# Optimization experiments

Measured on AMD Instinct MI355X. Metric: run time of the kernel, lower is better.

The kernel has to match this reference:

```python
import jax, jax.numpy as jnp
import numpy as np

IMG_LEN, TXT_LEN = 50, 76
SEQ = IMG_LEN + TXT_LEN
D_IMG, D, VOCAB = 768, 512, 49408
N_LAYERS = 2
EPS = 1e-5


def _layer_norm(x, g, b):
    m = jnp.mean(x, axis=-1, keepdims=True)
    v = jnp.mean(jnp.square(x - m), axis=-1, keepdims=True)
    return (x - m) * jax.lax.rsqrt(v + EPS) * g + b


def setup_inputs() -> dict:
    key = jax.random.key(0)
    ks = jax.random.split(key, 20)
    s = 0.02
    inp = {
        "image_embeddings": jax.random.normal(ks[0], (32, IMG_LEN, D_IMG), jnp.float32),
        "caption_ids": jax.random.randint(ks[1], (32, TXT_LEN), 0, VOCAB),
        "token_emb": jax.random.normal(ks[2], (VOCAB, D), jnp.float32) * s,
        "pos_emb": jax.random.normal(ks[3], (TXT_LEN, D), jnp.float32) * s,
        "ff0_w": jax.random.normal(ks[4], (D_IMG, D), jnp.float32) * s,
        "ff0_b": jnp.zeros((D,), jnp.float32),
        "wq": jax.random.normal(ks[5], (D, D), jnp.float32) * s,
        "wq_b": jnp.zeros((D,), jnp.float32),
        "wk": jax.random.normal(ks[6], (D, D), jnp.float32) * s,
        "wk_b": jnp.zeros((D,), jnp.float32),
        "wv": jax.random.normal(ks[7], (D, D), jnp.float32) * s,
        "wv_b": jnp.zeros((D,), jnp.float32),
        "ln_g": jnp.ones((D,), jnp.float32),
        "ln_b": jnp.zeros((D,), jnp.float32),
        "ff1_w": jax.random.normal(ks[8], (D, D), jnp.float32) * s,
        "ff1_b": jnp.zeros((D,), jnp.float32),
        "ff2_w": jax.random.normal(ks[9], (D, VOCAB), jnp.float32) * s,
        "ff2_b": jnp.zeros((VOCAB,), jnp.float32),
    }
    return inp


def reference(image_embeddings, caption_ids, token_emb, pos_emb, ff0_w, ff0_b,
              wq, wq_b, wk, wk_b, wv, wv_b, ln_g, ln_b, ff1_w, ff1_b, ff2_w, ff2_b):
    # prefix-causal mask: fully visible image prefix, causal over the rest
    mask = jnp.tril(jnp.ones((SEQ, SEQ), jnp.float32)).at[:, :IMG_LEN].set(1.0)

    img = image_embeddings @ ff0_w + ff0_b                      # [B,50,512]
    txt = token_emb[caption_ids] + pos_emb[None, :, :]          # [B,76,512]
    x = jnp.concatenate([img, txt], axis=1)                     # [B,126,512]
    x = _layer_norm(x, ln_g, ln_b)

    for _ in range(N_LAYERS):  # shared params across layers (as in source)
        res1 = x
        q = x @ wq + wq_b
        k = x @ wk + wk_b
        v = x @ wv + wv_b
        sims = jnp.einsum('bqd,bkd->bqk', q, k) / np.sqrt(D).astype(np.float32)
        sims = jnp.where(mask == 0, -1e9, sims)
        attn = jax.nn.softmax(sims, axis=-1)
        x = jnp.einsum('bqk,bkd->bqd', attn, v)
        x = _layer_norm(x + res1, ln_g, ln_b)
        res2 = x
        x = x @ ff1_w + ff1_b
        x = _layer_norm(x + res2, ln_g, ln_b)

    logits = x @ ff2_w + ff2_b                                  # [B,126,VOCAB]
    return logits[:, IMG_LEN:, :]                               # [B,76,VOCAB]
```

## Files before the change

kernel.cpp:

```cpp
#include <hip/hip_runtime.h>

typedef unsigned short ushort_t;
typedef __attribute__((ext_vector_type(8))) short short8;
typedef __attribute__((ext_vector_type(4))) float f32x4;
typedef __attribute__((ext_vector_type(4))) unsigned short bf4;
typedef __attribute__((ext_vector_type(8))) unsigned short bf8v;

__device__ __forceinline__ ushort_t f2bf(float f) {
    union { float f; unsigned u; } v; v.f = f;
    unsigned r = v.u + 0x7FFFu + ((v.u >> 16) & 1u);
    return (ushort_t)(r >> 16);
}

__device__ __forceinline__ void g2lds16(const ushort_t* g, ushort_t* l) {
    __builtin_amdgcn_global_load_lds(
        (const __attribute__((address_space(1))) void*)g,
        (__attribute__((address_space(3))) void*)l, 16, 0, 0);
}

#define LDT 72

__global__ __launch_bounds__(512) void gemm_big(
    const ushort_t* __restrict__ xb, const ushort_t* __restrict__ B,
    float* __restrict__ C, const float* __restrict__ bias,
    int K, int ldb, int ldc, int validM)
{
    __shared__ __attribute__((aligned(16))) ushort_t As[2][256 * 64];
    __shared__ __attribute__((aligned(16))) ushort_t Bs[2][256 * 64];

    const int tid = threadIdx.x;
    const int lane = tid & 63;
    const int wave = tid >> 6;
    const int wr = wave >> 2;
    const int wc = wave & 3;
    int tN, tM;
    {
        const int lin = blockIdx.x + blockIdx.y * gridDim.x;
        const int TM = gridDim.y;
        const int full = gridDim.x >> 3;
        const int per = TM << 3;
        const int g = lin / per;
        if (g < full) {
            const int rem = lin - g * per;
            tM = rem >> 3;
            tN = (g << 3) + (rem & 7);
        } else {
            const int rem = lin - full * per;
            const int w = gridDim.x - (full << 3);
            tM = rem / w;
            tN = (full << 3) + rem - tM * w;
        }
    }
    const int n0 = tN * 256;
    const ushort_t* Bbase = B + (long)n0 * ldb;

    f32x4 acc[8][4];
#pragma unroll
    for (int m = 0; m < 8; m++)
#pragma unroll
        for (int n = 0; n < 4; n++) acc[m][n] = (f32x4)0.f;

    auto STAGE = [&](int buf, int ks) {
#pragma unroll
        for (int i = 0; i < 4; i++) {
            int ch = i * 512 + tid;
            int row = ch >> 3, c16 = ch & 7;
            int c16s = c16 ^ (row & 7);
            int gr = tM * 256 + row;
            if (gr > 2431) gr = 2431;
            int bb = gr / 76;
            int xrow = bb * 126 + 50 + (gr - bb * 76);
            g2lds16(xb + (long)xrow * 512 + ks + (c16s << 3),
                    &As[buf][(i * 512 + wave * 64) * 8]);
        }
#pragma unroll
        for (int i = 0; i < 4; i++) {
            int ch = i * 512 + tid;
            int row = ch >> 3, c16 = ch & 7;
            int c16s = c16 ^ (row & 7);
            g2lds16(Bbase + (long)row * ldb + ks + (c16s << 3),
                    &Bs[buf][(i * 512 + wave * 64) * 8]);
        }
    };

    const int nt = K >> 6;
    STAGE(0, 0);
    for (int t = 0; t < nt; ++t) {
        if (t + 1 < nt) {
            STAGE((t + 1) & 1, (t + 1) << 6);
            asm volatile("s_waitcnt vmcnt(8)" ::: "memory");
        } else {
            asm volatile("s_waitcnt vmcnt(0)" ::: "memory");
        }
        asm volatile("s_barrier" ::: "memory");

        const ushort_t* Ac = As[t & 1];
        const ushort_t* Bc = Bs[t & 1];
        __builtin_amdgcn_s_setprio(1);
#pragma unroll
        for (int ksub = 0; ksub < 2; ksub++) {
            const int kk = ksub * 32 + ((lane >> 4) << 3);
            const int kc = kk >> 3;
            short8 af[8], bfr[4];
#pragma unroll
            for (int m = 0; m < 8; m++) {
                const int r = (wr << 7) + m * 16 + (lane & 15);
                af[m] = *(const short8*)(Ac + r * 64 + ((kc ^ (r & 7)) << 3));
            }
#pragma unroll
            for (int n = 0; n < 4; n++) {
                const int r = (wc << 6) + n * 16 + (lane & 15);
                bfr[n] = *(const short8*)(Bc + r * 64 + ((kc ^ (r & 7)) << 3));
            }
#pragma unroll
            for (int m = 0; m < 8; m++)
#pragma unroll
                for (int n = 0; n < 4; n++)
                    acc[m][n] = __builtin_amdgcn_mfma_f32_16x16x32_bf16(
                        af[m], bfr[n], acc[m][n], 0, 0, 0);
        }
        __builtin_amdgcn_s_setprio(0);
        asm volatile("s_barrier" ::: "memory");
    }

    const int rb = (wr << 7) + ((lane >> 4) << 2);
    const int cb = (wc << 6) + (lane & 15);
#pragma unroll
    for (int m = 0; m < 8; m++) {
#pragma unroll
        for (int i = 0; i < 4; i++) {
            int r = tM * 256 + rb + m * 16 + i;
            if (r >= validM) continue;
#pragma unroll
            for (int n = 0; n < 4; n++) {
                int cg = n0 + cb + n * 16;
                C[(long)r * ldc + cg] = acc[m][n][i] + bias[cg];
            }
        }
    }
}

__global__ __launch_bounds__(512) void attn_fused(
    const ushort_t* __restrict__ qkv, float* __restrict__ xg,
    ushort_t* __restrict__ xbg, const float* __restrict__ ln_g,
    const float* __restrict__ ln_b)
{
    __shared__ __attribute__((aligned(16))) ushort_t smem[41984];
    ushort_t* Vs = smem;
    ushort_t* Ps = smem + 32768;
    float* redm = (float*)(smem + 40960);
    float* reds = redm + 256;
    ushort_t* Qs = smem;
    ushort_t* Ks = smem + 8192;

    const int tid = threadIdx.x;
    const int lane = tid & 63;
    const int wave = tid >> 6;
    const int wr = wave >> 2;
    const int wc = wave & 3;
    const int qh = blockIdx.x;
    const int b  = blockIdx.y;
    const long qbase = ((long)(b * 126) + qh * 64) * 1536;
    const long kbase = (long)(b * 126) * 1536 + 512;
    const long vbase = (long)(b * 126) * 1536 + 1024;
    const float rsqd = 0.044194173824159216f;

    f32x4 acc[2][2];
#pragma unroll
    for (int m = 0; m < 2; m++)
#pragma unroll
        for (int n = 0; n < 2; n++) acc[m][n] = (f32x4)0.f;

    auto SQK = [&](int buf, int ks) {
        {
            int ch = tid;
            int row = ch >> 3, c16 = ch & 7;
            int c16s = c16 ^ (row & 7);
            g2lds16(qkv + qbase + (long)row * 1536 + ks + (c16s << 3),
                    Qs + buf * 4096 + (wave * 64) * 8);
        }
#pragma unroll
        for (int i = 0; i < 2; i++) {
            int ch = i * 512 + tid;
            int row = ch >> 3, c16 = ch & 7;
            int c16s = c16 ^ (row & 7);
            g2lds16(qkv + kbase + (long)row * 1536 + ks + (c16s << 3),
                    Ks + buf * 8192 + (i * 512 + wave * 64) * 8);
        }
    };

    SQK(0, 0);
    for (int t = 0; t < 8; ++t) {
        if (t < 7) {
            SQK((t + 1) & 1, (t + 1) << 6);
            asm volatile("s_waitcnt vmcnt(3)" ::: "memory");
        } else {
            asm volatile("s_waitcnt vmcnt(0)" ::: "memory");
        }
        asm volatile("s_barrier" ::: "memory");
        const ushort_t* Qc = Qs + (t & 1) * 4096;
        const ushort_t* Kc = Ks + (t & 1) * 8192;
#pragma unroll
        for (int ksub = 0; ksub < 2; ksub++) {
            const int kc = ksub * 4 + (lane >> 4);
            short8 af[2], bfr[2];
#pragma unroll
            for (int m = 0; m < 2; m++) {
                const int r = (wr << 5) + m * 16 + (lane & 15);
                af[m] = *(const short8*)(Qc + r * 64 + ((kc ^ (r & 7)) << 3));
            }
#pragma unroll
            for (int n = 0; n < 2; n++) {
                const int r = (wc << 5) + n * 16 + (lane & 15);
                bfr[n] = *(const short8*)(Kc + r * 64 + ((kc ^ (r & 7)) << 3));
            }
#pragma unroll
            for (int m = 0; m < 2; m++)
#pragma unroll
                for (int n = 0; n < 2; n++)
                    acc[m][n] = __builtin_amdgcn_mfma_f32_16x16x32_bf16(
                        af[m], bfr[n], acc[m][n], 0, 0, 0);
        }
        asm volatile("s_barrier" ::: "memory");
    }

    float rm[2][4];
#pragma unroll
    for (int m = 0; m < 2; m++) {
#pragma unroll
        for (int i = 0; i < 4; i++) {
            const int rl = (wr << 5) + m * 16 + ((lane >> 4) << 2) + i;
            const int q = qh * 64 + rl;
            float mx = -3.0e38f;
#pragma unroll
            for (int n = 0; n < 2; n++) {
                int j = (wc << 5) + n * 16 + (lane & 15);
                bool ok = (j < 126) && ((j < 50) || (j <= q));
                float s = acc[m][n][i] * rsqd;
                acc[m][n][i] = ok ? s : -3.0e38f;
                if (ok) mx = fmaxf(mx, s);
            }
#pragma unroll
            for (int o = 8; o >= 1; o >>= 1) mx = fmaxf(mx, __shfl_xor(mx, o));
            rm[m][i] = mx;
        }
    }
    if ((lane & 15) == 0) {
#pragma unroll
        for (int m = 0; m < 2; m++)
#pragma unroll
            for (int i = 0; i < 4; i++) {
                int rl = (wr << 5) + m * 16 + ((lane >> 4) << 2) + i;
                redm[wc * 64 + rl] = rm[m][i];
            }
    }
    __syncthreads();
    float rs[2][4];
#pragma unroll
    for (int m = 0; m < 2; m++) {
#pragma unroll
        for (int i = 0; i < 4; i++) {
            const int rl = (wr << 5) + m * 16 + ((lane >> 4) << 2) + i;
            float M = fmaxf(fmaxf(redm[rl], redm[64 + rl]),
                            fmaxf(redm[128 + rl], redm[192 + rl]));
            float sum = 0.f;
#pragma unroll
            for (int n = 0; n < 2; n++) {
                float s = acc[m][n][i];
                float e = (s > -1.0e37f) ? expf(s - M) : 0.f;
                acc[m][n][i] = e;
                sum += e;
            }
#pragma unroll
            for (int o = 8; o >= 1; o >>= 1) sum += __shfl_xor(sum, o);
            rs[m][i] = sum;
        }
    }
    if ((lane & 15) == 0) {
#pragma unroll
        for (int m = 0; m < 2; m++)
#pragma unroll
            for (int i = 0; i < 4; i++) {
                int rl = (wr << 5) + m * 16 + ((lane >> 4) << 2) + i;
                reds[wc * 64 + rl] = rs[m][i];
            }
    }
    __syncthreads();
#pragma unroll
    for (int m = 0; m < 2; m++) {
#pragma unroll
        for (int i = 0; i < 4; i++) {
            const int rl = (wr << 5) + m * 16 + ((lane >> 4) << 2) + i;
            float S = reds[rl] + reds[64 + rl] + reds[128 + rl] + reds[192 + rl];
            float inv = 1.f / S;
#pragma unroll
            for (int n = 0; n < 2; n++) {
                int j = (wc << 5) + n * 16 + (lane & 15);
                int c = j >> 3;
                Ps[rl * 128 + ((c ^ (rl & 7)) << 3) + (j & 7)] =
                    f2bf(acc[m][n][i] * inv);
            }
        }
    }
    __syncthreads();

    f32x4 po[2][8];
#pragma unroll
    for (int m = 0; m < 2; m++)
#pragma unroll
        for (int n = 0; n < 8; n++) po[m][n] = (f32x4)0.f;

    for (int jc = 0; jc < 2; jc++) {
#pragma unroll
        for (int q8 = 0; q8 < 16; q8++) {
            int qid = q8 * 512 + tid;
            int d = qid & 511, jq = qid >> 9;
            const ushort_t* vp = qkv + vbase + (long)(jc * 64 + jq * 4) * 1536 + d;
            bf4 p;
            p[0] = vp[0];
            p[1] = vp[1536];
            p[2] = vp[3072];
            p[3] = vp[4608];
            *(bf4*)(Vs + d * 64 + (((jq >> 1) ^ (d & 7)) << 3) + ((jq & 1) << 2)) = p;
        }
        __syncthreads();
#pragma unroll
        for (int ksub = 0; ksub < 2; ksub++) {
            const int kc = ksub * 4 + (lane >> 4);
            short8 af[2], bv[8];
#pragma unroll
            for (int m = 0; m < 2; m++) {
                const int r = (wr << 5) + m * 16 + (lane & 15);
                const int c = jc * 8 + kc;
                af[m] = *(const short8*)(Ps + r * 128 + ((c ^ (r & 7)) << 3));
            }
#pragma unroll
            for (int n = 0; n < 8; n++) {
                const int r = (wc << 7) + n * 16 + (lane & 15);
                bv[n] = *(const short8*)(Vs + r * 64 + ((kc ^ (r & 7)) << 3));
            }
#pragma unroll
            for (int m = 0; m < 2; m++)
#pragma unroll
                for (int n = 0; n < 8; n++)
                    po[m][n] = __builtin_amdgcn_mfma_f32_16x16x32_bf16(
                        af[m], bv[n], po[m][n], 0, 0, 0);
        }
        __syncthreads();
    }

    float gg[8], bb2[8];
#pragma unroll
    for (int n = 0; n < 8; n++) {
        int d = (wc << 7) + n * 16 + (lane & 15);
        gg[n] = ln_g[d];
        bb2[n] = ln_b[d];
    }
#pragma unroll
    for (int m = 0; m < 2; m++) {
#pragma unroll
        for (int i = 0; i < 4; i++) {
            const int rl = (wr << 5) + m * 16 + ((lane >> 4) << 2) + i;
            const int q = qh * 64 + rl;
            const long xrow = ((long)(b * 126 + q)) << 9;
            float s = 0.f, sq = 0.f;
#pragma unroll
            for (int n = 0; n < 8; n++) {
                int d = (wc << 7) + n * 16 + (lane & 15);
                float v = po[m][n][i] + xg[xrow + d];
                po[m][n][i] = v;
                s += v; sq += v * v;
            }
#pragma unroll
            for (int o = 8; o >= 1; o >>= 1) { s += __shfl_xor(s, o); sq += __shfl_xor(sq, o); }
            if ((lane & 15) == 0) {
                redm[wc * 64 + rl] = s;
                reds[wc * 64 + rl] = sq;
            }
        }
    }
    __syncthreads();
#pragma unroll
    for (int m = 0; m < 2; m++) {
#pragma unroll
        for (int i = 0; i < 4; i++) {
            const int rl = (wr << 5) + m * 16 + ((lane >> 4) << 2) + i;
            const int q = qh * 64 + rl;
            if (q >= 126) continue;
            float S = redm[rl] + redm[64 + rl] + redm[128 + rl] + redm[192 + rl];
            float SQ = reds[rl] + reds[64 + rl] + reds[128 + rl] + reds[192 + rl];
            float mean = S * (1.f / 512.f);
            float var = SQ * (1.f / 512.f) - mean * mean;
            float inv = rsqrtf(var + 1e-5f);
            const long xrow = ((long)(b * 126 + q)) << 9;
#pragma unroll
            for (int n = 0; n < 8; n++) {
                int d = (wc << 7) + n * 16 + (lane & 15);
                float y = (po[m][n][i] - mean) * inv * gg[n] + bb2[n];
                xg[xrow + d] = y;
                xbg[xrow + d] = f2bf(y);
            }
        }
    }
}

template <int BSRC, int SWZ, int NT>
__global__ __launch_bounds__(256) void gemm_bf16(
    const ushort_t* __restrict__ A, const void* __restrict__ Bv,
    float* __restrict__ C, ushort_t* __restrict__ Cb,
    const float* __restrict__ bias,
    int K, int lda, int ldb, int ldc,
    long sA, long sB, long sC,
    int validM, float scale)
{
    constexpr int LS = (BSRC == 0) ? 64 : LDT;
    constexpr int NBUF = (BSRC == 0) ? 2 : 1;
    __shared__ __attribute__((aligned(16))) ushort_t As[NBUF * 128 * LS];
    __shared__ __attribute__((aligned(16))) ushort_t Bs[NBUF * 128 * LS];

    const int tid = threadIdx.x;
    const int lane = tid & 63;
    const int wave = tid >> 6;
    const int wr = wave >> 1, wc = wave & 1;
    int tN = blockIdx.x, tM = blockIdx.y;
    const int bz = blockIdx.z;
    if (SWZ) {
        const int lin = blockIdx.x + blockIdx.y * gridDim.x;
        const int TM = gridDim.y;
        const int full = gridDim.x >> 3;
        const int per = TM << 3;
        const int g = lin / per;
        if (g < full) {
            const int rem = lin - g * per;
            tM = rem >> 3;
            tN = (g << 3) + (rem & 7);
        } else {
            const int rem = lin - full * per;
            const int w = gridDim.x - (full << 3);
            tM = rem / w;
            tN = (full << 3) + rem - tM * w;
        }
    }
    const int n0 = tN * 128;

    const ushort_t* Abase = A + (long)bz * sA + (long)tM * 128 * lda;
    const ushort_t* Bb = (BSRC == 0)
        ? (const ushort_t*)Bv + (long)bz * sB + (long)n0 * ldb : nullptr;
    const float* Bf = (BSRC == 1)
        ? (const float*)Bv + (long)bz * sB : nullptr;

    f32x4 acc[4][4];
#pragma unroll
    for (int m = 0; m < 4; m++)
#pragma unroll
        for (int n = 0; n < 4; n++) acc[m][n] = (f32x4)0.f;

    if (BSRC == 0) {
        auto STAGE = [&](int buf, int ks) {
            ushort_t* Ad = As + buf * (128 * 64);
            ushort_t* Bd = Bs + buf * (128 * 64);
#pragma unroll
            for (int i = 0; i < 4; i++) {
                int ch = wave * 256 + i * 64 + lane;
                int row = ch >> 3, c16 = ch & 7;
                int c16s = c16 ^ (row & 7);
                g2lds16(Abase + (long)row * lda + ks + (c16s << 3),
                        Ad + (wave * 256 + i * 64) * 8);
            }
#pragma unroll
            for (int i = 0; i < 4; i++) {
                int ch = wave * 256 + i * 64 + lane;
                int row = ch >> 3, c16 = ch & 7;
                int c16s = c16 ^ (row & 7);
                g2lds16(Bb + (long)row * ldb + ks + (c16s << 3),
                        Bd + (wave * 256 + i * 64) * 8);
            }
        };

        const int nt = K >> 6;
        STAGE(0, 0);
        for (int t = 0; t < nt; ++t) {
            if (t + 1 < nt) {
                STAGE((t + 1) & 1, (t + 1) << 6);
                asm volatile("s_waitcnt vmcnt(8)" ::: "memory");
            } else {
                asm volatile("s_waitcnt vmcnt(0)" ::: "memory");
            }
            asm volatile("s_barrier" ::: "memory");

            const ushort_t* Ac = As + (t & 1) * (128 * 64);
            const ushort_t* Bc = Bs + (t & 1) * (128 * 64);
#pragma unroll
            for (int ksub = 0; ksub < 2; ksub++) {
                const int kk = ksub * 32 + ((lane >> 4) << 3);
                const int kc = kk >> 3;
                short8 af[4], bfr[4];
#pragma unroll
                for (int m = 0; m < 4; m++) {
                    const int r = (wr << 6) + m * 16 + (lane & 15);
                    af[m] = *(const short8*)(Ac + r * 64 + ((kc ^ (r & 7)) << 3));
                }
#pragma unroll
                for (int n = 0; n < 4; n++) {
                    const int r = (wc << 6) + n * 16 + (lane & 15);
                    bfr[n] = *(const short8*)(Bc + r * 64 + ((kc ^ (r & 7)) << 3));
                }
#pragma unroll
                for (int m = 0; m < 4; m++)
#pragma unroll
                    for (int n = 0; n < 4; n++)
                        acc[m][n] = __builtin_amdgcn_mfma_f32_16x16x32_bf16(
                            af[m], bfr[n], acc[m][n], 0, 0, 0);
            }
            asm volatile("s_barrier" ::: "memory");
        }
    } else {
        for (int ks = 0; ks < K; ks += 64) {
            short8 ar[4];
#pragma unroll
            for (int i = 0; i < 4; i++) {
                int ch = wave * 256 + i * 64 + lane;
                int row = ch >> 3, c16 = ch & 7;
                ar[i] = *(const short8*)(Abase + (long)row * lda + ks + (c16 << 3));
            }
            bf4 pk[8];
#pragma unroll
            for (int q = 0; q < 8; q++) {
                int qid = q * 256 + tid;
                int n = qid & 127, kq = qid >> 7;
                const float* wp = Bf + (long)(ks + kq * 4) * ldb + n0 + n;
                bf4 p;
                p[0] = f2bf(wp[0]);
                p[1] = f2bf(wp[ldb]);
                p[2] = f2bf(wp[2 * (long)ldb]);
                p[3] = f2bf(wp[3 * (long)ldb]);
                pk[q] = p;
            }
            if (ks) __syncthreads();
#pragma unroll
            for (int i = 0; i < 4; i++) {
                int ch = wave * 256 + i * 64 + lane;
                int row = ch >> 3, c16 = ch & 7;
                *(short8*)(As + row * LS + (c16 << 3)) = ar[i];
            }
#pragma unroll
            for (int q = 0; q < 8; q++) {
                int qid = q * 256 + tid;
                int n = qid & 127, kq = qid >> 7;
                *(bf4*)(Bs + n * LS + (kq << 2)) = pk[q];
            }
            __syncthreads();

#pragma unroll
            for (int ksub = 0; ksub < 2; ksub++) {
                const int kk = ksub * 32 + ((lane >> 4) << 3);
                short8 af[4], bfr[4];
#pragma unroll
                for (int m = 0; m < 4; m++) {
                    const int r = (wr << 6) + m * 16 + (lane & 15);
                    af[m] = *(const short8*)(As + r * LS + kk);
                }
#pragma unroll
                for (int n = 0; n < 4; n++) {
                    const int r = (wc << 6) + n * 16 + (lane & 15);
                    bfr[n] = *(const short8*)(Bs + r * LS + kk);
                }
#pragma unroll
                for (int m = 0; m < 4; m++)
#pragma unroll
                    for (int n = 0; n < 4; n++)
                        acc[m][n] = __builtin_amdgcn_mfma_f32_16x16x32_bf16(
                            af[m], bfr[n], acc[m][n], 0, 0, 0);
            }
            if (ks + 64 < K) __syncthreads();
        }
    }

    const int rb = (wr << 6) + ((lane >> 4) << 2);
    const int cb = (wc << 6) + (lane & 15);
#pragma unroll
    for (int m = 0; m < 4; m++) {
#pragma unroll
        for (int i = 0; i < 4; i++) {
            int r = tM * 128 + rb + m * 16 + i;
            if (r >= validM) continue;
#pragma unroll
            for (int n = 0; n < 4; n++) {
                int cg = n0 + cb + n * 16;
                float v = acc[m][n][i] * scale + (bias ? bias[cg] : 0.f);
                long off = (long)bz * sC + (long)r * ldc + cg;
                if (C) {
                    if (NT) __builtin_nontemporal_store(v, &C[off]);
                    else    C[off] = v;
                }
                if (Cb) Cb[off] = f2bf(v);
            }
        }
    }
}

__global__ __launch_bounds__(256) void transpose_bf(
    const float* __restrict__ in, ushort_t* __restrict__ out, int R, int C)
{
    __shared__ float t[32][33];
    int c0 = blockIdx.x << 5, r0 = blockIdx.y << 5;
    int tx = threadIdx.x, ty = threadIdx.y;
#pragma unroll
    for (int i = 0; i < 4; i++)
        t[ty + i * 8][tx] = in[(long)(r0 + ty + i * 8) * C + c0 + tx];
    __syncthreads();
#pragma unroll
    for (int i = 0; i < 4; i++)
        out[(long)(c0 + ty + i * 8) * R + r0 + tx] = f2bf(t[tx][ty + i * 8]);
}

__global__ __launch_bounds__(256) void transpose_bf3(
    const float* __restrict__ s0, const float* __restrict__ s1,
    const float* __restrict__ s2, ushort_t* __restrict__ out)
{
    __shared__ float t[32][33];
    const float* in = (blockIdx.z == 0) ? s0 : (blockIdx.z == 1) ? s1 : s2;
    ushort_t* o = out + (long)blockIdx.z * 512 * 512;
    int c0 = blockIdx.x << 5, r0 = blockIdx.y << 5;
    int tx = threadIdx.x, ty = threadIdx.y;
#pragma unroll
    for (int i = 0; i < 4; i++)
        t[ty + i * 8][tx] = in[(long)(r0 + ty + i * 8) * 512 + c0 + tx];
    __syncthreads();
#pragma unroll
    for (int i = 0; i < 4; i++)
        o[(long)(c0 + ty + i * 8) * 512 + r0 + tx] = f2bf(t[tx][ty + i * 8]);
}

__global__ __launch_bounds__(256) void biascat(
    const float* __restrict__ b0, const float* __restrict__ b1,
    const float* __restrict__ b2, float* __restrict__ out)
{
    int i = blockIdx.x * 256 + threadIdx.x;
    const float* s = (i < 512) ? b0 : (i < 1024) ? b1 : b2;
    out[i] = s[i & 511];
}

__global__ __launch_bounds__(256) void conv_pad(
    const float* __restrict__ in, ushort_t* __restrict__ out,
    int validR, int C, int total)
{
    int idx = blockIdx.x * 256 + threadIdx.x;
    if (idx >= total) return;
    int r = idx / C;
    float v = 0.f;
    if (r < validR) v = in[idx];
    out[idx] = f2bf(v);
}

__global__ __launch_bounds__(256) void gather_txt(
    const ushort_t* __restrict__ xb, ushort_t* __restrict__ At)
{
    int idx = blockIdx.x * 256 + threadIdx.x;
    if (idx >= 2560 * 512) return;
    int r = idx >> 9, c = idx & 511;
    if (r < 2432) {
        int b = r / 76, t = r - b * 76;
        At[idx] = xb[((long)(b * 126 + 50 + t) << 9) + c];
    } else {
        At[idx] = 0;
    }
}

__global__ __launch_bounds__(64) void build_x(
    const float* __restrict__ imgout, const int* __restrict__ cap,
    const float* __restrict__ tok, const float* __restrict__ pos,
    const float* __restrict__ g, const float* __restrict__ bb,
    float* __restrict__ x, ushort_t* __restrict__ xb)
{
    int r = blockIdx.x, lane = threadIdx.x;
    int c0 = lane << 3;
    long base = ((long)r << 9) + c0;
    if (r >= 4032) {
        *(f32x4*)(x + base) = (f32x4)0.f;
        *(f32x4*)(x + base + 4) = (f32x4)0.f;
        *(bf8v*)(xb + base) = (bf8v)0;
        return;
    }
    int b = r / 126, s = r - b * 126;
    float v[8];
    if (s < 50) {
        const float* src = imgout + ((long)(b * 50 + s) << 9) + c0;
        f32x4 a0 = *(const f32x4*)src, a1 = *(const f32x4*)(src + 4);
#pragma unroll
        for (int i = 0; i < 4; i++) { v[i] = a0[i]; v[4 + i] = a1[i]; }
    } else {
        int t = s - 50;
        int id = cap[b * 76 + t];
        const float* s1 = tok + ((long)id << 9) + c0;
        const float* s2 = pos + ((long)t << 9) + c0;
        f32x4 a0 = *(const f32x4*)s1, a1 = *(const f32x4*)(s1 + 4);
        f32x4 b0 = *(const f32x4*)s2, b1 = *(const f32x4*)(s2 + 4);
#pragma unroll
        for (int i = 0; i < 4; i++) { v[i] = a0[i] + b0[i]; v[4 + i] = a1[i] + b1[i]; }
    }
    float sum = 0.f, sq = 0.f;
#pragma unroll
    for (int i = 0; i < 8; i++) { sum += v[i]; sq += v[i] * v[i]; }
#pragma unroll
    for (int o = 32; o >= 1; o >>= 1) { sum += __shfl_xor(sum, o); sq += __shfl_xor(sq, o); }
    float mean = sum * (1.f / 512.f);
    float var = sq * (1.f / 512.f) - mean * mean;
    float inv = rsqrtf(var + 1e-5f);
    bf8v ob;
#pragma unroll
    for (int i = 0; i < 8; i++) {
        float y = (v[i] - mean) * inv * g[c0 + i] + bb[c0 + i];
        x[base + i] = y;
        ob[i] = f2bf(y);
    }
    *(bf8v*)(xb + base) = ob;
}

__global__ __launch_bounds__(64) void resln(
    const float* __restrict__ a, const float* __restrict__ g,
    const float* __restrict__ bb, float* __restrict__ x, ushort_t* __restrict__ xb)
{
    int r = blockIdx.x, lane = threadIdx.x;
    int c0 = lane << 3;
    long base = ((long)r << 9) + c0;
    if (r >= 4032) {
        *(f32x4*)(x + base) = (f32x4)0.f;
        *(f32x4*)(x + base + 4) = (f32x4)0.f;
        *(bf8v*)(xb + base) = (bf8v)0;
        return;
    }
    f32x4 a0 = *(const f32x4*)(a + base), a1 = *(const f32x4*)(a + base + 4);
    f32x4 x0 = *(const f32x4*)(x + base), x1 = *(const f32x4*)(x + base + 4);
    float v[8];
#pragma unroll
    for (int i = 0; i < 4; i++) { v[i] = a0[i] + x0[i]; v[4 + i] = a1[i] + x1[i]; }
    float sum = 0.f, sq = 0.f;
#pragma unroll
    for (int i = 0; i < 8; i++) { sum += v[i]; sq += v[i] * v[i]; }
#pragma unroll
    for (int o = 32; o >= 1; o >>= 1) { sum += __shfl_xor(sum, o); sq += __shfl_xor(sq, o); }
    float mean = sum * (1.f / 512.f);
    float var = sq * (1.f / 512.f) - mean * mean;
    float inv = rsqrtf(var + 1e-5f);
    bf8v ob;
#pragma unroll
    for (int i = 0; i < 8; i++) {
        float y = (v[i] - mean) * inv * g[c0 + i] + bb[c0 + i];
        x[base + i] = y;
        ob[i] = f2bf(y);
    }
    *(bf8v*)(xb + base) = ob;
}

extern "C" void kernel_launch(void* const* d_in, const int* in_sizes, int n_in,
                              void* d_out, int out_size, void* d_ws, size_t ws_size,
                              hipStream_t stream)
{
    const float* img   = (const float*)d_in[0];
    const int*   cap   = (const int*)  d_in[1];
    const float* tok   = (const float*)d_in[2];
    const float* pos   = (const float*)d_in[3];
    const float* ff0_w = (const float*)d_in[4];
    const float* ff0_b = (const float*)d_in[5];
    const float* wq    = (const float*)d_in[6];
    const float* wq_b  = (const float*)d_in[7];
    const float* wk    = (const float*)d_in[8];
    const float* wk_b  = (const float*)d_in[9];
    const float* wv    = (const float*)d_in[10];
    const float* wv_b  = (const float*)d_in[11];
    const float* ln_g  = (const float*)d_in[12];
    const float* ln_b  = (const float*)d_in[13];
    const float* ff1_w = (const float*)d_in[14];
    const float* ff1_b = (const float*)d_in[15];
    const float* ff2_w = (const float*)d_in[16];
    const float* ff2_b = (const float*)d_in[17];

    char* ws = (char*)d_ws;
    size_t o = 0;
    auto alloc = [&](size_t bytes) { size_t r = o; o += (bytes + 255) & ~(size_t)255; return r; };

    float*    x     = (float*)   (ws + alloc(4096ull * 512 * 4));
    ushort_t* xb    = (ushort_t*)(ws + alloc(4096ull * 512 * 2));
    float*    tmpf  = (float*)   (ws + alloc(4096ull * 512 * 4));
    ushort_t* qkvb  = (ushort_t*)(ws + alloc(4096ull * 1536 * 2));
    ushort_t* Atxt  = (ushort_t*)(ws + alloc(2560ull * 512 * 2));
    ushort_t* Aimg  = (ushort_t*)(ws + alloc(1664ull * 768 * 2));
    ushort_t* wqkvT = (ushort_t*)(ws + alloc(1536ull * 512 * 2));
    ushort_t* ff0T  = (ushort_t*)(ws + alloc(512ull * 768 * 2));
    ushort_t* ff1T  = (ushort_t*)(ws + alloc(512ull * 512 * 2));
    float*    bcat  = (float*)   (ws + alloc(1536 * 4));
    size_t base_bytes = o;
    size_t ff2T_bytes = 49408ull * 512 * 2;
    bool use_ff2T = (ws_size >= base_bytes + ff2T_bytes + 256);
    ushort_t* ff2T = use_ff2T ? (ushort_t*)(ws + alloc(ff2T_bytes)) : nullptr;

    dim3 b32x8(32, 8);

    transpose_bf3<<<dim3(16, 16, 3), b32x8, 0, stream>>>(wq, wk, wv, wqkvT);
    transpose_bf<<<dim3(16, 24), b32x8, 0, stream>>>(ff0_w, ff0T, 768, 512);
    transpose_bf<<<dim3(16, 16), b32x8, 0, stream>>>(ff1_w, ff1T, 512, 512);
    biascat<<<6, 256, 0, stream>>>(wq_b, wk_b, wv_b, bcat);
    if (use_ff2T)
        transpose_bf<<<dim3(1544, 16), b32x8, 0, stream>>>(ff2_w, ff2T, 512, 49408);
    conv_pad<<<(1664 * 768 + 255) / 256, 256, 0, stream>>>(img, Aimg, 1600, 768, 1664 * 768);

    gemm_bf16<0, 0, 0><<<dim3(4, 13, 1), 256, 0, stream>>>(
        Aimg, ff0T, tmpf, nullptr, ff0_b, 768, 768, 768, 512, 0, 0, 0, 1600, 1.f);

    build_x<<<4096, 64, 0, stream>>>(tmpf, cap, tok, pos, ln_g, ln_b, x, xb);

    for (int l = 0; l < 2; l++) {
        gemm_bf16<0, 0, 0><<<dim3(12, 32, 1), 256, 0, stream>>>(
            xb, wqkvT, nullptr, qkvb, bcat, 512, 512, 512, 1536, 0, 0, 0, 4096, 1.f);
        attn_fused<<<dim3(2, 32), 512, 0, stream>>>(qkvb, x, xb, ln_g, ln_b);
        gemm_bf16<0, 0, 0><<<dim3(4, 32, 1), 256, 0, stream>>>(
            xb, ff1T, tmpf, nullptr, ff1_b, 512, 512, 512, 512, 0, 0, 0, 4032, 1.f);
        resln<<<4096, 64, 0, stream>>>(tmpf, ln_g, ln_b, x, xb);
    }

    if (use_ff2T) {
        gemm_big<<<dim3(193, 10), 512, 0, stream>>>(
            xb, ff2T, (float*)d_out, ff2_b, 512, 512, 49408, 2432);
    } else {
        gather_txt<<<(2560 * 512 + 255) / 256, 256, 0, stream>>>(xb, Atxt);
        gemm_bf16<1, 1, 0><<<dim3(386, 20, 1), 256, 0, stream>>>(
            Atxt, ff2_w, (float*)d_out, nullptr, ff2_b, 512, 512, 49408, 49408,
            0, 0, 0, 2432, 1.f);
    }
}
```

Before: 456.0 us.

## Fuse ff1 GEMM with residual add and layernorm into one kernel

Replaces the ff1 GEMM, which wrote fp32 to a temp buffer, and the separate residual+layernorm kernel with a single kernel. Each 512-thread block computes 32 full rows of 512 columns with MFMA, then adds bias and the residual and applies layernorm through a shared-memory cross-wave reduction. This removes one launch and the temp-buffer round trip per layer. In exchange it uses only 126 blocks, runs a single-buffered K loop, and every block re-reads the whole ff1 weight.

```diff
diff --git a/kernel.cpp b/kernel.cpp
--- a/kernel.cpp
+++ b/kernel.cpp
@@ -140,6 +140,125 @@
     }
 }
 
+__global__ __launch_bounds__(512) void ff1_fused(
+    ushort_t* __restrict__ xbg, const ushort_t* __restrict__ ff1T,
+    const float* __restrict__ bias, float* __restrict__ xg,
+    const float* __restrict__ ln_g, const float* __restrict__ ln_b)
+{
+    __shared__ __attribute__((aligned(16))) ushort_t As[32 * 64];
+    __shared__ __attribute__((aligned(16))) ushort_t Bs[512 * 64];
+    __shared__ float redm[4 * 32];
+    __shared__ float reds[4 * 32];
+
+    const int tid = threadIdx.x;
+    const int lane = tid & 63;
+    const int wave = tid >> 6;
+    const int wr = wave >> 2;
+    const int wc = wave & 3;
+    const int r0 = blockIdx.x << 5;
+
+    f32x4 acc[8];
+#pragma unroll
+    for (int n = 0; n < 8; n++) acc[n] = (f32x4)0.f;
+
+    auto STAGE = [&](int ks) {
+#pragma unroll
+        for (int i = 0; i < 9; i++) {
+            int cb = i * 512 + wave * 64;
+            if (cb >= 4352) continue;
+            int ch = cb + lane;
+            if (cb < 256) {
+                int row = ch >> 3, c16 = ch & 7;
+                int c16s = c16 ^ (row & 7);
+                g2lds16(xbg + (long)(r0 + row) * 512 + ks + (c16s << 3),
+                        &As[cb * 8]);
+            } else {
+                int bch = ch - 256;
+                int row = bch >> 3, c16 = bch & 7;
+                int c16s = c16 ^ (row & 7);
+                g2lds16(ff1T + (long)row * 512 + ks + (c16s << 3),
+                        &Bs[(cb - 256) * 8]);
+            }
+        }
+    };
+
+    for (int ks = 0; ks < 512; ks += 64) {
+        if (ks) asm volatile("s_barrier" ::: "memory");
+        STAGE(ks);
+        asm volatile("s_waitcnt vmcnt(0)" ::: "memory");
+        asm volatile("s_barrier" ::: "memory");
+
+        __builtin_amdgcn_s_setprio(1);
+#pragma unroll
+        for (int ksub = 0; ksub < 2; ksub++) {
+            const int kc = ksub * 4 + (lane >> 4);
+            short8 af;
+            {
+                const int r = (wr << 4) + (lane & 15);
+                af = *(const short8*)(As + r * 64 + ((kc ^ (r & 7)) << 3));
+            }
+            short8 bfr[8];
+#pragma unroll
+            for (int n = 0; n < 8; n++) {
+                const int r = (wc << 7) + n * 16 + (lane & 15);
+                bfr[n] = *(const short8*)(Bs + r * 64 + ((kc ^ (r & 7)) << 3));
+            }
+#pragma unroll
+            for (int n = 0; n < 8; n++)
+                acc[n] = __builtin_amdgcn_mfma_f32_16x16x32_bf16(
+                    af, bfr[n], acc[n], 0, 0, 0);
+        }
+        __builtin_amdgcn_s_setprio(0);
+    }
+
+    float gg[8], bb2[8], bi[8];
+#pragma unroll
+    for (int n = 0; n < 8; n++) {
+        int d = (wc << 7) + n * 16 + (lane & 15);
+        gg[n] = ln_g[d];
+        bb2[n] = ln_b[d];
+        bi[n] = bias[d];
+    }
+    float vv[4][8];
+#pragma unroll
+    for (int i = 0; i < 4; i++) {
+        const int rl = (wr << 4) + ((lane >> 4) << 2) + i;
+        const long xrow = (long)(r0 + rl) << 9;
+        float s = 0.f, sq = 0.f;
+#pragma unroll
+        for (int n = 0; n < 8; n++) {
+            int d = (wc << 7) + n * 16 + (lane & 15);
+            float v = acc[n][i] + bi[n] + xg[xrow + d];
+            vv[i][n] = v;
+            s += v; sq += v * v;
+        }
+#pragma unroll
+        for (int o = 8; o >= 1; o >>= 1) { s += __shfl_xor(s, o); sq += __shfl_xor(sq, o); }
+        if ((lane & 15) == 0) {
+            redm[wc * 32 + rl] = s;
+            reds[wc * 32 + rl] = sq;
+        }
+    }
+    __syncthreads();
+#pragma unroll
+    for (int i = 0; i < 4; i++) {
+        const int rl = (wr << 4) + ((lane >> 4) << 2) + i;
+        float S = redm[rl] + redm[32 + rl] + redm[64 + rl] + redm[96 + rl];
+        float SQ = reds[rl] + reds[32 + rl] + reds[64 + rl] + reds[96 + rl];
+        float mean = S * (1.f / 512.f);
+        float var = SQ * (1.f / 512.f) - mean * mean;
+        float inv = rsqrtf(var + 1e-5f);
+        const long xrow = (long)(r0 + rl) << 9;
+#pragma unroll
+        for (int n = 0; n < 8; n++) {
+            int d = (wc << 7) + n * 16 + (lane & 15);
+            float y = (vv[i][n] - mean) * inv * gg[n] + bb2[n];
+            xg[xrow + d] = y;
+            xbg[xrow + d] = f2bf(y);
+        }
+    }
+}
+
 __global__ __launch_bounds__(512) void attn_fused(
     const ushort_t* __restrict__ qkv, float* __restrict__ xg,
     ushort_t* __restrict__ xbg, const float* __restrict__ ln_g,
@@ -717,42 +836,6 @@
     *(bf8v*)(xb + base) = ob;
 }
 
-__global__ __launch_bounds__(64) void resln(
-    const float* __restrict__ a, const float* __restrict__ g,
-    const float* __restrict__ bb, float* __restrict__ x, ushort_t* __restrict__ xb)
-{
-    int r = blockIdx.x, lane = threadIdx.x;
-    int c0 = lane << 3;
-    long base = ((long)r << 9) + c0;
-    if (r >= 4032) {
-        *(f32x4*)(x + base) = (f32x4)0.f;
-        *(f32x4*)(x + base + 4) = (f32x4)0.f;
-        *(bf8v*)(xb + base) = (bf8v)0;
-        return;
-    }
-    f32x4 a0 = *(const f32x4*)(a + base), a1 = *(const f32x4*)(a + base + 4);
-    f32x4 x0 = *(const f32x4*)(x + base), x1 = *(const f32x4*)(x + base + 4);
-    float v[8];
-#pragma unroll
-    for (int i = 0; i < 4; i++) { v[i] = a0[i] + x0[i]; v[4 + i] = a1[i] + x1[i]; }
-    float sum = 0.f, sq = 0.f;
-#pragma unroll
-    for (int i = 0; i < 8; i++) { sum += v[i]; sq += v[i] * v[i]; }
-#pragma unroll
-    for (int o = 32; o >= 1; o >>= 1) { sum += __shfl_xor(sum, o); sq += __shfl_xor(sq, o); }
-    float mean = sum * (1.f / 512.f);
-    float var = sq * (1.f / 512.f) - mean * mean;
-    float inv = rsqrtf(var + 1e-5f);
-    bf8v ob;
-#pragma unroll
-    for (int i = 0; i < 8; i++) {
-        float y = (v[i] - mean) * inv * g[c0 + i] + bb[c0 + i];
-        x[base + i] = y;
-        ob[i] = f2bf(y);
-    }
-    *(bf8v*)(xb + base) = ob;
-}
-
 extern "C" void kernel_launch(void* const* d_in, const int* in_sizes, int n_in,
                               void* d_out, int out_size, void* d_ws, size_t ws_size,
                               hipStream_t stream)
@@ -814,9 +897,7 @@
         gemm_bf16<0, 0, 0><<<dim3(12, 32, 1), 256, 0, stream>>>(
             xb, wqkvT, nullptr, qkvb, bcat, 512, 512, 512, 1536, 0, 0, 0, 4096, 1.f);
         attn_fused<<<dim3(2, 32), 512, 0, stream>>>(qkvb, x, xb, ln_g, ln_b);
-        gemm_bf16<0, 0, 0><<<dim3(4, 32, 1), 256, 0, stream>>>(
-            xb, ff1T, tmpf, nullptr, ff1_b, 512, 512, 512, 512, 0, 0, 0, 4032, 1.f);
-        resln<<<4096, 64, 0, stream>>>(tmpf, ln_g, ln_b, x, xb);
+        ff1_fused<<<126, 512, 0, stream>>>(xb, ff1T, ff1_b, x, ln_g, ln_b);
     }
 
     if (use_ff2T) {
```

New measurement: 441.6 us. -3.2%, faster.
